# Kernel tuning notes

Hardware: AMD Instinct MI355X
Metric: run time of the kernel (lower is better)

The kernel has to match this reference:

```python
import jax, jax.numpy as jnp
import numpy as np

B, D, K = 8192, 512, 4096
MAX_WORD_LENGTH = 16
RESIDUAL_THRESHOLD = 0.01
DECAY_FACTOR = 0.95
EPS_TARGET = 1e-8


def setup_inputs() -> dict:
    key = jax.random.key(0)
    k1, k2 = jax.random.split(key)
    targets = jax.random.normal(k1, (B, D), dtype=jnp.float32)
    codebook = jax.random.normal(k2, (K, D), dtype=jnp.float32)
    return {"targets": targets, "codebook": codebook}


def reference(targets, codebook):
    """Batched greedy residual pursuit (allow_negative_signs=True).

    Returns:
      seq      [B, L] int32 signed indices (>=0: add idx; <0: subtract (-idx-1)); 0 where inactive
      mask     [B, L] bool, True where a step actually emitted a symbol
      residual [B, D] final residual after pursuit
    """
    target_norm = jnp.linalg.norm(targets, axis=-1)  # [B]

    def step(residual, step_idx):
        rnorm = jnp.linalg.norm(residual, axis=-1)  # [B]
        active = (rnorm >= RESIDUAL_THRESHOLD) & (target_norm >= EPS_TARGET)
        # cosine similarity of each codebook vector with residual direction
        res_dir = residual / jnp.maximum(rnorm, 1e-12)[:, None]
        cos = jnp.einsum('bd,kd->bk', res_dir, codebook)  # [B, K]
        best = jnp.argmax(jnp.abs(cos), axis=-1)  # [B]
        best_cos = jnp.take_along_axis(cos, best[:, None], axis=-1)[:, 0]
        signed = jnp.where(best_cos >= 0, best, -(best + 1)).astype(jnp.int32)
        sign = jnp.where(best_cos >= 0, 1.0, -1.0).astype(residual.dtype)
        decay = jnp.power(jnp.asarray(DECAY_FACTOR, residual.dtype),
                          (step_idx + 1).astype(residual.dtype))
        contrib = sign[:, None] * decay * codebook[best]  # [B, D]
        new_res = jnp.where(active[:, None], residual - contrib, residual)
        out_idx = jnp.where(active, signed, 0)
        return new_res, (out_idx, active)

    residual, (seq, mask) = jax.lax.scan(step, targets, jnp.arange(MAX_WORD_LENGTH))
    return seq.T, mask.T, residual
```

## Files before the change

### kernel.cpp

```cpp
#include <hip/hip_runtime.h>
#include <hip/hip_bf16.h>

#define B_SZ 8192
#define D_SZ 512
#define K_SZ 4096
#define L_SZ 16
#define M_ALL (B_SZ + K_SZ)

typedef __attribute__((ext_vector_type(8))) short short8v;
typedef __attribute__((ext_vector_type(4))) float f32x4;
typedef _Float16 half8v __attribute__((ext_vector_type(8)));

__global__ void cast_bf16_kernel(const float* __restrict__ targets,
                                 const float* __restrict__ codebook,
                                 __hip_bfloat16* __restrict__ abf) {
    int idx = blockIdx.x * blockDim.x + threadIdx.x;
    const int total4 = (M_ALL * D_SZ) / 4;
    if (idx >= total4) return;
    int base = idx * 4;
    const float* src = (base < B_SZ * D_SZ) ? (targets + base)
                                            : (codebook + (base - B_SZ * D_SZ));
    float4 v = *(const float4*)src;
    abf[base + 0] = __float2bfloat16(v.x);
    abf[base + 1] = __float2bfloat16(v.y);
    abf[base + 2] = __float2bfloat16(v.z);
    abf[base + 3] = __float2bfloat16(v.w);
}

__global__ void cn2_kernel(const float* __restrict__ codebook,
                           double* __restrict__ cn2) {
    int row  = blockIdx.x * 4 + (threadIdx.x >> 6);
    int lane = threadIdx.x & 63;
    const float* r = codebook + (size_t)row * D_SZ;
    double s = 0.0;
#pragma unroll
    for (int j = 0; j < 8; j++) { double v = (double)r[lane + 64 * j]; s += v * v; }
#pragma unroll
    for (int o = 32; o > 0; o >>= 1) s += __shfl_down(s, o, 64);
    if (lane == 0) cn2[row] = s;
}

#define BM 128
#define BN 128
#define BK 32
#define LDSS 40

__global__ __launch_bounds__(256, 2)
void gemm_bt_kernel(const __hip_bfloat16* __restrict__ A,
                    const __hip_bfloat16* __restrict__ Bm,
                    _Float16* __restrict__ C) {
    __shared__ short As[BM * LDSS];
    __shared__ short Bs[BN * LDSS];
    const int tid  = threadIdx.x;
    const int bm   = blockIdx.y * BM;
    const int bn   = blockIdx.x * BN;
    const int wave = tid >> 6, lane = tid & 63;
    const int wm = (wave & 1) * 64, wn = (wave >> 1) * 64;
    const int row16 = lane & 15, quad = lane >> 4;
    const int koff = quad * 8;

    f32x4 acc[4][4] = {};

    const int srow = tid >> 1;
    const int scol = (tid & 1) * 16;
    const short* Ag = (const short*)A;
    const short* Bg = (const short*)Bm;

    for (int k0 = 0; k0 < D_SZ; k0 += BK) {
        short8v a0 = *(const short8v*)(Ag + (size_t)(bm + srow) * D_SZ + k0 + scol);
        short8v a1 = *(const short8v*)(Ag + (size_t)(bm + srow) * D_SZ + k0 + scol + 8);
        short8v b0 = *(const short8v*)(Bg + (size_t)(bn + srow) * D_SZ + k0 + scol);
        short8v b1 = *(const short8v*)(Bg + (size_t)(bn + srow) * D_SZ + k0 + scol + 8);
        __syncthreads();
        *(short8v*)(As + srow * LDSS + scol)     = a0;
        *(short8v*)(As + srow * LDSS + scol + 8) = a1;
        *(short8v*)(Bs + srow * LDSS + scol)     = b0;
        *(short8v*)(Bs + srow * LDSS + scol + 8) = b1;
        __syncthreads();

        short8v af[4], bf[4];
#pragma unroll
        for (int i = 0; i < 4; i++)
            af[i] = *(const short8v*)(As + (wm + i * 16 + row16) * LDSS + koff);
#pragma unroll
        for (int j = 0; j < 4; j++)
            bf[j] = *(const short8v*)(Bs + (wn + j * 16 + row16) * LDSS + koff);
#pragma unroll
        for (int i = 0; i < 4; i++)
#pragma unroll
            for (int j = 0; j < 4; j++)
                acc[i][j] = __builtin_amdgcn_mfma_f32_16x16x32_bf16(af[i], bf[j], acc[i][j], 0, 0, 0);
    }

#pragma unroll
    for (int i = 0; i < 4; i++) {
        int grow = bm + wm + i * 16 + quad * 4;
#pragma unroll
        for (int j = 0; j < 4; j++) {
            int gcol = bn + wn + j * 16 + row16;
#pragma unroll
            for (int r = 0; r < 4; r++)
                C[(size_t)(grow + r) * K_SZ + gcol] = (_Float16)acc[i][j][r];
        }
    }
}

#define MAXC 32
#define MARGIN 1.0f

__global__ __launch_bounds__(256, 4)
void pursuit_kernel(const float* __restrict__ targets,
                    const float* __restrict__ codebook,
                    const _Float16* __restrict__ S,
                    const double* __restrict__ cn2,
                    float* __restrict__ out) {
    const int wave = threadIdx.x >> 6;
    const int lane = threadIdx.x & 63;
    const int b = blockIdx.x * 4 + wave;
    const int lane8 = lane * 8;

    __shared__ int s_cnt[4];
    __shared__ int s_cand[4][MAXC];
    int* cnt  = &s_cnt[wave];
    int* cand = s_cand[wave];

    float g_r[64];
    {
        const _Float16* g0 = S + (size_t)b * K_SZ + lane8;
#pragma unroll
        for (int jb = 0; jb < 8; jb++) {
            half8v h = *(const half8v*)(g0 + jb * 512);
#pragma unroll
            for (int e = 0; e < 8; e++) g_r[jb * 8 + e] = (float)h[e];
        }
    }

    double rres[8];
    double loc = 0.0;
    {
        const float* tg = targets + (size_t)b * D_SZ + lane8;
        float4 t0 = *(const float4*)tg;
        float4 t1 = *(const float4*)(tg + 4);
        rres[0] = t0.x; rres[1] = t0.y; rres[2] = t0.z; rres[3] = t0.w;
        rres[4] = t1.x; rres[5] = t1.y; rres[6] = t1.z; rres[7] = t1.w;
#pragma unroll
        for (int e = 0; e < 8; e++) loc += rres[e] * rres[e];
    }
#pragma unroll
    for (int o = 32; o > 0; o >>= 1) loc += __shfl_xor(loc, o, 64);
    const double tn2 = loc;
    double rn2 = tn2;
    const bool tgt_ok = (sqrt(tn2) >= 1e-8);

    float* out_seq  = out;
    float* out_mask = out + (size_t)B_SZ * L_SZ;
    float* out_res  = out + (size_t)2 * B_SZ * L_SZ;

    double decay = 1.0;
    for (int t = 0; t < L_SZ; t++) {
        decay *= 0.95;
        bool active = (sqrt(rn2) >= 0.01) && tgt_ok;
        if (!active) {
            if (lane == 0) {
                out_seq[(size_t)b * L_SZ + t]  = 0.0f;
                out_mask[(size_t)b * L_SZ + t] = 0.0f;
            }
            continue;
        }

        float m = 0.0f;
#pragma unroll
        for (int j = 0; j < 64; j++) m = fmaxf(m, fabsf(g_r[j]));
        float M = m;
#pragma unroll
        for (int o = 32; o > 0; o >>= 1) M = fmaxf(M, __shfl_xor(M, o, 64));
        float thr = M - MARGIN;

        if (lane == 0) *cnt = 0;
        if (m >= thr) {
#pragma unroll
            for (int jb = 0; jb < 8; jb++)
#pragma unroll
                for (int e = 0; e < 8; e++)
                    if (fabsf(g_r[jb * 8 + e]) >= thr) {
                        int p = atomicAdd(cnt, 1);
                        if (p < MAXC) cand[p] = jb * 512 + lane8 + e;
                    }
        }
        __threadfence_block();
        int nc = min(*cnt, MAXC);

        int bk = -1; double bv = 0.0; bool have = false;
        for (int ci = 0; ci < nc; ci++) {
            int k = cand[ci];
            const float* crow = codebook + (size_t)k * D_SZ + lane8;
            float4 c0 = *(const float4*)crow;
            float4 c1 = *(const float4*)(crow + 4);
            double s = rres[0] * (double)c0.x + rres[1] * (double)c0.y
                     + rres[2] * (double)c0.z + rres[3] * (double)c0.w
                     + rres[4] * (double)c1.x + rres[5] * (double)c1.y
                     + rres[6] * (double)c1.z + rres[7] * (double)c1.w;
#pragma unroll
            for (int o = 32; o > 0; o >>= 1) s += __shfl_xor(s, o, 64);
            if (!have || fabs(s) > fabs(bv) ||
                (fabs(s) == fabs(bv) && k < bk)) { bk = k; bv = s; have = true; }
        }

        double sd = ((bv >= 0.0) ? 1.0 : -1.0) * decay;
        rn2 = rn2 - 2.0 * sd * bv + sd * sd * cn2[bk];
        if (lane == 0) {
            out_seq[(size_t)b * L_SZ + t]  = (float)((bv >= 0.0) ? bk : (-bk - 1));
            out_mask[(size_t)b * L_SZ + t] = 1.0f;
        }
        const float sdf = (float)sd;

        const _Float16* Grow = S + (size_t)(B_SZ + bk) * K_SZ + lane8;
#pragma unroll
        for (int jb = 0; jb < 8; jb++) {
            half8v h = *(const half8v*)(Grow + jb * 512);
#pragma unroll
            for (int e = 0; e < 8; e++) g_r[jb * 8 + e] -= sdf * (float)h[e];
        }
        const float* crow = codebook + (size_t)bk * D_SZ + lane8;
        {
            float4 c0 = *(const float4*)crow;
            float4 c1 = *(const float4*)(crow + 4);
            rres[0] -= sd * (double)c0.x; rres[1] -= sd * (double)c0.y;
            rres[2] -= sd * (double)c0.z; rres[3] -= sd * (double)c0.w;
            rres[4] -= sd * (double)c1.x; rres[5] -= sd * (double)c1.y;
            rres[6] -= sd * (double)c1.z; rres[7] -= sd * (double)c1.w;
        }
    }

    {
        float* o = out_res + (size_t)b * D_SZ + lane8;
        float4 r0, r1;
        r0.x = (float)rres[0]; r0.y = (float)rres[1]; r0.z = (float)rres[2]; r0.w = (float)rres[3];
        r1.x = (float)rres[4]; r1.y = (float)rres[5]; r1.z = (float)rres[6]; r1.w = (float)rres[7];
        *(float4*)o = r0;
        *(float4*)(o + 4) = r1;
    }
}

extern "C" void kernel_launch(void* const* d_in, const int* in_sizes, int n_in,
                              void* d_out, int out_size, void* d_ws, size_t ws_size,
                              hipStream_t stream) {
    const float* targets  = (const float*)d_in[0];
    const float* codebook = (const float*)d_in[1];
    float* out = (float*)d_out;

    __hip_bfloat16* abf = (__hip_bfloat16*)d_ws;
    _Float16* S = (_Float16*)((char*)d_ws + (size_t)M_ALL * D_SZ * 2);
    double* cn2 = (double*)((char*)d_ws + (size_t)M_ALL * D_SZ * 2
                                        + (size_t)M_ALL * K_SZ * 2);

    int total4 = (M_ALL * D_SZ) / 4;
    cast_bf16_kernel<<<(total4 + 255) / 256, 256, 0, stream>>>(targets, codebook, abf);
    cn2_kernel<<<K_SZ / 4, 256, 0, stream>>>(codebook, cn2);

    dim3 ggrid(K_SZ / BN, M_ALL / BM);
    gemm_bt_kernel<<<ggrid, 256, 0, stream>>>(abf, abf + (size_t)B_SZ * D_SZ, S);

    pursuit_kernel<<<B_SZ / 4, 256, 0, stream>>>(targets, codebook, S, cn2, out);
}
```

Measured before the change: 382.8 us.

## Pack pursuit scores as half2, move residual to LDS, fast-path single candidate

The pursuit kernel now keeps its per-lane score vector as packed fp16 pairs and does the max and update with packed half ops. The double-precision residual moves from registers into shared memory, and launch bounds rise to 8 blocks per SM to raise occupancy. A single-candidate fast path prefetches the chosen codebook and Gram rows early. The selected entry's score is overwritten with its exactly computed value, and the step loop exits early once a row goes inactive. The costs are fp16 accumulation drift in the scores, a tighter candidate cap (MAXC 16) with a wider margin, and extra LDS traffic for the residual.

```diff
diff --git a/kernel.cpp b/kernel.cpp
--- a/kernel.cpp
+++ b/kernel.cpp
@@ -10,6 +10,20 @@
 typedef __attribute__((ext_vector_type(8))) short short8v;
 typedef __attribute__((ext_vector_type(4))) float f32x4;
 typedef _Float16 half8v __attribute__((ext_vector_type(8)));
+typedef _Float16 h2 __attribute__((ext_vector_type(2)));
+struct H2x4 { h2 a, b, c, d; };
+
+static __device__ __forceinline__ h2 habs2(h2 a) {
+    unsigned u = __builtin_bit_cast(unsigned, a) & 0x7FFF7FFFu;
+    return __builtin_bit_cast(h2, u);
+}
+static __device__ __forceinline__ h2 hmax2(h2 a, h2 b) {
+#if __has_builtin(__builtin_elementwise_max)
+    return __builtin_elementwise_max(a, b);
+#else
+    h2 r; r[0] = a[0] > b[0] ? a[0] : b[0]; r[1] = a[1] > b[1] ? a[1] : b[1]; return r;
+#endif
+}
 
 __global__ void cast_bf16_kernel(const float* __restrict__ targets,
                                  const float* __restrict__ codebook,
@@ -105,10 +119,10 @@
     }
 }
 
-#define MAXC 32
-#define MARGIN 1.0f
-
-__global__ __launch_bounds__(256, 4)
+#define MAXC 16
+#define MARGIN 1.25f
+
+__global__ __launch_bounds__(256, 8)
 void pursuit_kernel(const float* __restrict__ targets,
                     const float* __restrict__ codebook,
                     const _Float16* __restrict__ S,
@@ -119,58 +133,70 @@
     const int b = blockIdx.x * 4 + wave;
     const int lane8 = lane * 8;
 
+    __shared__ double rres_s[4][D_SZ];
     __shared__ int s_cnt[4];
     __shared__ int s_cand[4][MAXC];
+    double* rres = rres_s[wave];
     int* cnt  = &s_cnt[wave];
     int* cand = s_cand[wave];
 
-    float g_r[64];
+#define RL(e) rres[(e) * 64 + lane]
+
+    h2 g2[32];
     {
         const _Float16* g0 = S + (size_t)b * K_SZ + lane8;
 #pragma unroll
         for (int jb = 0; jb < 8; jb++) {
-            half8v h = *(const half8v*)(g0 + jb * 512);
-#pragma unroll
-            for (int e = 0; e < 8; e++) g_r[jb * 8 + e] = (float)h[e];
-        }
-    }
-
-    double rres[8];
+            H2x4 u = __builtin_bit_cast(H2x4, *(const half8v*)(g0 + jb * 512));
+            g2[jb * 4 + 0] = u.a; g2[jb * 4 + 1] = u.b;
+            g2[jb * 4 + 2] = u.c; g2[jb * 4 + 3] = u.d;
+        }
+    }
+
     double loc = 0.0;
     {
         const float* tg = targets + (size_t)b * D_SZ + lane8;
         float4 t0 = *(const float4*)tg;
         float4 t1 = *(const float4*)(tg + 4);
-        rres[0] = t0.x; rres[1] = t0.y; rres[2] = t0.z; rres[3] = t0.w;
-        rres[4] = t1.x; rres[5] = t1.y; rres[6] = t1.z; rres[7] = t1.w;
-#pragma unroll
-        for (int e = 0; e < 8; e++) loc += rres[e] * rres[e];
+        RL(0) = t0.x; RL(1) = t0.y; RL(2) = t0.z; RL(3) = t0.w;
+        RL(4) = t1.x; RL(5) = t1.y; RL(6) = t1.z; RL(7) = t1.w;
+        loc = (double)t0.x * t0.x + (double)t0.y * t0.y + (double)t0.z * t0.z
+            + (double)t0.w * t0.w + (double)t1.x * t1.x + (double)t1.y * t1.y
+            + (double)t1.z * t1.z + (double)t1.w * t1.w;
     }
 #pragma unroll
     for (int o = 32; o > 0; o >>= 1) loc += __shfl_xor(loc, o, 64);
-    const double tn2 = loc;
-    double rn2 = tn2;
-    const bool tgt_ok = (sqrt(tn2) >= 1e-8);
-
-    float* out_seq  = out;
-    float* out_mask = out + (size_t)B_SZ * L_SZ;
-    float* out_res  = out + (size_t)2 * B_SZ * L_SZ;
-
+    double rn2 = loc;
+    const bool tgt_ok = (sqrt(loc) >= 1e-8);
+
+    float* out_seq  = out + (size_t)b * L_SZ;
+    float* out_mask = out + (size_t)B_SZ * L_SZ + (size_t)b * L_SZ;
+    float* out_res  = out + (size_t)2 * B_SZ * L_SZ + (size_t)b * D_SZ;
+
+    auto lanemax = [&]() -> float {
+        h2 t[16];
+#pragma unroll
+        for (int j = 0; j < 16; j++) t[j] = hmax2(habs2(g2[j]), habs2(g2[j + 16]));
+#pragma unroll
+        for (int j = 0; j < 8; j++)  t[j] = hmax2(t[j], t[j + 8]);
+#pragma unroll
+        for (int j = 0; j < 4; j++)  t[j] = hmax2(t[j], t[j + 4]);
+        h2 f = hmax2(hmax2(t[0], t[1]), hmax2(t[2], t[3]));
+        return fmaxf((float)f[0], (float)f[1]);
+    };
+
+    float m = lanemax();
     double decay = 1.0;
+
     for (int t = 0; t < L_SZ; t++) {
         decay *= 0.95;
         bool active = (sqrt(rn2) >= 0.01) && tgt_ok;
         if (!active) {
-            if (lane == 0) {
-                out_seq[(size_t)b * L_SZ + t]  = 0.0f;
-                out_mask[(size_t)b * L_SZ + t] = 0.0f;
-            }
-            continue;
-        }
-
-        float m = 0.0f;
-#pragma unroll
-        for (int j = 0; j < 64; j++) m = fmaxf(m, fabsf(g_r[j]));
+            if (lane == 0)
+                for (int tt = t; tt < L_SZ; tt++) { out_seq[tt] = 0.0f; out_mask[tt] = 0.0f; }
+            break;
+        }
+
         float M = m;
 #pragma unroll
         for (int o = 32; o > 0; o >>= 1) M = fmaxf(M, __shfl_xor(M, o, 64));
@@ -179,67 +205,119 @@
         if (lane == 0) *cnt = 0;
         if (m >= thr) {
 #pragma unroll
-            for (int jb = 0; jb < 8; jb++)
-#pragma unroll
-                for (int e = 0; e < 8; e++)
-                    if (fabsf(g_r[jb * 8 + e]) >= thr) {
-                        int p = atomicAdd(cnt, 1);
-                        if (p < MAXC) cand[p] = jb * 512 + lane8 + e;
-                    }
+            for (int p = 0; p < 32; p++) {
+                float f0 = (float)g2[p][0], f1 = (float)g2[p][1];
+                int kbase = (p >> 2) * 512 + lane8 + ((p & 3) * 2);
+                if (fabsf(f0) >= thr) { int q = atomicAdd(cnt, 1); if (q < MAXC) cand[q] = kbase; }
+                if (fabsf(f1) >= thr) { int q = atomicAdd(cnt, 1); if (q < MAXC) cand[q] = kbase + 1; }
+            }
         }
         __threadfence_block();
         int nc = min(*cnt, MAXC);
 
-        int bk = -1; double bv = 0.0; bool have = false;
-        for (int ci = 0; ci < nc; ci++) {
-            int k = cand[ci];
-            const float* crow = codebook + (size_t)k * D_SZ + lane8;
-            float4 c0 = *(const float4*)crow;
-            float4 c1 = *(const float4*)(crow + 4);
-            double s = rres[0] * (double)c0.x + rres[1] * (double)c0.y
-                     + rres[2] * (double)c0.z + rres[3] * (double)c0.w
-                     + rres[4] * (double)c1.x + rres[5] * (double)c1.y
-                     + rres[6] * (double)c1.z + rres[7] * (double)c1.w;
+        int bk; double bv;
+        float4 c0, c1;
+        half8v Ga, Gb;
+        const _Float16* Gp;
+
+        if (nc == 1) {
+            bk = __builtin_amdgcn_readfirstlane(cand[0]);
+            const float* cr = codebook + (size_t)bk * D_SZ + lane8;
+            Gp = S + (size_t)(B_SZ + bk) * K_SZ + lane8;
+            c0 = *(const float4*)cr;
+            c1 = *(const float4*)(cr + 4);
+            Ga = *(const half8v*)(Gp);
+            Gb = *(const half8v*)(Gp + 512);
+            double s = RL(0) * (double)c0.x + RL(1) * (double)c0.y
+                     + RL(2) * (double)c0.z + RL(3) * (double)c0.w
+                     + RL(4) * (double)c1.x + RL(5) * (double)c1.y
+                     + RL(6) * (double)c1.z + RL(7) * (double)c1.w;
 #pragma unroll
             for (int o = 32; o > 0; o >>= 1) s += __shfl_xor(s, o, 64);
-            if (!have || fabs(s) > fabs(bv) ||
-                (fabs(s) == fabs(bv) && k < bk)) { bk = k; bv = s; have = true; }
-        }
-
+            bv = s;
+        } else {
+            bk = -1; bv = 0.0;
+            for (int ci = 0; ci < nc; ci++) {
+                int k = __builtin_amdgcn_readfirstlane(cand[ci]);
+                const float* cr = codebook + (size_t)k * D_SZ + lane8;
+                float4 d0 = *(const float4*)cr;
+                float4 d1 = *(const float4*)(cr + 4);
+                double s = RL(0) * (double)d0.x + RL(1) * (double)d0.y
+                         + RL(2) * (double)d0.z + RL(3) * (double)d0.w
+                         + RL(4) * (double)d1.x + RL(5) * (double)d1.y
+                         + RL(6) * (double)d1.z + RL(7) * (double)d1.w;
+#pragma unroll
+                for (int o = 32; o > 0; o >>= 1) s += __shfl_xor(s, o, 64);
+                if (bk < 0 || fabs(s) > fabs(bv) ||
+                    (fabs(s) == fabs(bv) && k < bk)) { bk = k; bv = s; }
+            }
+            const float* cr = codebook + (size_t)bk * D_SZ + lane8;
+            Gp = S + (size_t)(B_SZ + bk) * K_SZ + lane8;
+            c0 = *(const float4*)cr;
+            c1 = *(const float4*)(cr + 4);
+            Ga = *(const half8v*)(Gp);
+            Gb = *(const half8v*)(Gp + 512);
+        }
+
+        const double cn2bk = cn2[bk];
         double sd = ((bv >= 0.0) ? 1.0 : -1.0) * decay;
-        rn2 = rn2 - 2.0 * sd * bv + sd * sd * cn2[bk];
+        rn2 = rn2 - 2.0 * sd * bv + sd * sd * cn2bk;
         if (lane == 0) {
-            out_seq[(size_t)b * L_SZ + t]  = (float)((bv >= 0.0) ? bk : (-bk - 1));
-            out_mask[(size_t)b * L_SZ + t] = 1.0f;
+            out_seq[t]  = (float)((bv >= 0.0) ? bk : (-bk - 1));
+            out_mask[t] = 1.0f;
         }
         const float sdf = (float)sd;
-
-        const _Float16* Grow = S + (size_t)(B_SZ + bk) * K_SZ + lane8;
-#pragma unroll
-        for (int jb = 0; jb < 8; jb++) {
-            half8v h = *(const half8v*)(Grow + jb * 512);
-#pragma unroll
-            for (int e = 0; e < 8; e++) g_r[jb * 8 + e] -= sdf * (float)h[e];
-        }
-        const float* crow = codebook + (size_t)bk * D_SZ + lane8;
+        h2 sdh2; sdh2[0] = (_Float16)sdf; sdh2[1] = (_Float16)sdf;
+
+#pragma unroll
+        for (int jb = 0; jb < 8; jb += 2) {
+            half8v Gc, Gd;
+            if (jb + 2 < 8) {
+                Gc = *(const half8v*)(Gp + (jb + 2) * 512);
+                Gd = *(const half8v*)(Gp + (jb + 3) * 512);
+            }
+            H2x4 ua = __builtin_bit_cast(H2x4, Ga);
+            H2x4 ub = __builtin_bit_cast(H2x4, Gb);
+            g2[jb * 4 + 0] -= sdh2 * ua.a; g2[jb * 4 + 1] -= sdh2 * ua.b;
+            g2[jb * 4 + 2] -= sdh2 * ua.c; g2[jb * 4 + 3] -= sdh2 * ua.d;
+            g2[jb * 4 + 4] -= sdh2 * ub.a; g2[jb * 4 + 5] -= sdh2 * ub.b;
+            g2[jb * 4 + 6] -= sdh2 * ub.c; g2[jb * 4 + 7] -= sdh2 * ub.d;
+            Ga = Gc; Gb = Gd;
+        }
+
         {
-            float4 c0 = *(const float4*)crow;
-            float4 c1 = *(const float4*)(crow + 4);
-            rres[0] -= sd * (double)c0.x; rres[1] -= sd * (double)c0.y;
-            rres[2] -= sd * (double)c0.z; rres[3] -= sd * (double)c0.w;
-            rres[4] -= sd * (double)c1.x; rres[5] -= sd * (double)c1.y;
-            rres[6] -= sd * (double)c1.z; rres[7] -= sd * (double)c1.w;
-        }
+            float pf = (float)(bv - sd * cn2bk);
+            int rloc = bk & 511;
+            int lown = rloc >> 3;
+            int eo   = rloc & 7;
+            int pown = (bk >> 9) * 4 + (eo >> 1);
+#pragma unroll
+            for (int p = 0; p < 32; p++)
+                if (p == pown) {
+                    if (lane == lown) {
+                        h2 v = g2[p];
+                        if ((eo & 1) == 0) v[0] = (_Float16)pf; else v[1] = (_Float16)pf;
+                        g2[p] = v;
+                    }
+                }
+        }
+
+        RL(0) -= sd * (double)c0.x; RL(1) -= sd * (double)c0.y;
+        RL(2) -= sd * (double)c0.z; RL(3) -= sd * (double)c0.w;
+        RL(4) -= sd * (double)c1.x; RL(5) -= sd * (double)c1.y;
+        RL(6) -= sd * (double)c1.z; RL(7) -= sd * (double)c1.w;
+
+        m = lanemax();
     }
 
     {
-        float* o = out_res + (size_t)b * D_SZ + lane8;
         float4 r0, r1;
-        r0.x = (float)rres[0]; r0.y = (float)rres[1]; r0.z = (float)rres[2]; r0.w = (float)rres[3];
-        r1.x = (float)rres[4]; r1.y = (float)rres[5]; r1.z = (float)rres[6]; r1.w = (float)rres[7];
-        *(float4*)o = r0;
-        *(float4*)(o + 4) = r1;
-    }
+        r0.x = (float)RL(0); r0.y = (float)RL(1); r0.z = (float)RL(2); r0.w = (float)RL(3);
+        r1.x = (float)RL(4); r1.y = (float)RL(5); r1.z = (float)RL(6); r1.w = (float)RL(7);
+        *(float4*)(out_res + lane8) = r0;
+        *(float4*)(out_res + lane8 + 4) = r1;
+    }
+#undef RL
 }
 
 extern "C" void kernel_launch(void* const* d_in, const int* in_sizes, int n_in,
```

Result: slower. 727.7 us (+90.1%).
